# Performance work log

Measured on AMD Instinct MI355X. Metric: run time of the kernel, lower is better.

## Reference

```python
import jax, jax.numpy as jnp
import numpy as np

NUM_EMB = 8192
EMB_DIM = 512
SPAN = 8            # max_span == fixed_segment_size
COMMIT = 0.25
BOUND_W = 0.01


def setup_inputs() -> dict:
    key = jax.random.key(0)
    k_x, k_e, k_w = jax.random.split(key, 3)
    B, T, D = 16, 8192, EMB_DIM
    x = jax.random.normal(k_x, (B, T, D), dtype=jnp.float32)
    emb = jax.random.normal(k_e, (NUM_EMB, D), dtype=jnp.float32) * 0.02
    Wb = jax.random.normal(k_w, (D, 1), dtype=jnp.float32) * 0.02
    bb = jnp.zeros((1,), dtype=jnp.float32)
    return {"x": x, "emb": emb, "Wb": Wb, "bb": bb}


def reference(x, emb, Wb, bb):
    # Eval-mode forward of AdaptiveTemporalVQ (no gumbel sampling, no EMA update).
    B, T, D = x.shape
    # boundary predictor: Linear(D, 1) -> squeeze
    boundary_logits = (x @ Wb)[..., 0] + bb[0]                      # [B, T]
    boundaries = (jax.nn.sigmoid(boundary_logits) > 0.5).astype(x.dtype)

    num_segments = (T + SPAN - 1) // SPAN
    pad = num_segments * SPAN - T
    x_p = jnp.pad(x, ((0, 0), (0, pad), (0, 0))) if pad > 0 else x
    # temporal mean pooling over fixed segments
    pooled = x_p.reshape(B, num_segments, SPAN, D).mean(axis=2)      # [B, S, D]

    # --- VectorQuantizer ---
    flat = pooled.reshape(-1, D)                                     # [N, D]
    dist = (jnp.sum(flat ** 2, axis=1, keepdims=True)
            + jnp.sum(emb ** 2, axis=1)
            - 2.0 * flat @ emb.T)                                    # [N, K]
    idx = jnp.argmin(dist, axis=1)                                   # [N]
    quantized = emb[idx].reshape(B, num_segments, D)                 # codebook gather

    e_latent_loss = jnp.mean((jax.lax.stop_gradient(quantized) - pooled) ** 2)
    vq_loss = COMMIT * e_latent_loss
    # straight-through estimator
    q_st = pooled + jax.lax.stop_gradient(quantized - pooled)

    # expand each segment code back over its SPAN timesteps
    q_exp = jnp.broadcast_to(q_st[:, :, None, :], (B, num_segments, SPAN, D))
    quantized_out = q_exp.reshape(B, num_segments * SPAN, D)[:, :T, :]
    idx_seg = idx.reshape(B, num_segments)
    idx_out = jnp.broadcast_to(idx_seg[:, :, None], (B, num_segments, SPAN))
    idx_out = idx_out.reshape(B, num_segments * SPAN)[:, :T]

    target_rate = jnp.float32(1.0 / SPAN)
    boundary_loss = (boundaries.mean() - target_rate) ** 2
    total_loss = vq_loss + BOUND_W * boundary_loss
    return quantized_out, total_loss, idx_out, boundaries
```

## Files before the change

### kernel.cpp

```cpp
#include <hip/hip_runtime.h>

#define B_    16
#define T_    8192
#define D_    512
#define K_    8192
#define S_    1024
#define N_    16384
#define NBT   131072

#define LOSS_OFF 67108864
#define IDX_OFF  67108865
#define BND_OFF  67239937

typedef __bf16 bf16x8 __attribute__((ext_vector_type(8)));
typedef float  f32x4  __attribute__((ext_vector_type(4)));

__device__ __forceinline__ unsigned int fsort(float f){
  unsigned int u = __float_as_uint(f);
  return (u & 0x80000000u) ? ~u : (u | 0x80000000u);
}
__device__ __forceinline__ float funsort(unsigned int su){
  unsigned int u = (su & 0x80000000u) ? (su ^ 0x80000000u) : ~su;
  return __uint_as_float(u);
}
__device__ __forceinline__ unsigned short f2bf(float f){
  unsigned int u = __float_as_uint(f);
  return (unsigned short)((u + 0x7fffu + ((u >> 16) & 1u)) >> 16);
}
__device__ __forceinline__ void gload16(const void* g, void* l){
  __builtin_amdgcn_global_load_lds((const __attribute__((address_space(1))) void*)g,
                                   (__attribute__((address_space(3))) void*)l, 16, 0, 0);
}

#define VMW12() asm volatile("s_waitcnt vmcnt(12)" ::: "memory")
#define VMW8()  asm volatile("s_waitcnt vmcnt(8)"  ::: "memory")
#define VMW4()  asm volatile("s_waitcnt vmcnt(4)"  ::: "memory")
#define VMW0()  asm volatile("s_waitcnt vmcnt(0)"  ::: "memory")
#define LGKW()  asm volatile("s_waitcnt lgkmcnt(0)" ::: "memory")
#define BAR()   asm volatile("s_barrier" ::: "memory")

__global__ void k_embnorm(const float4* __restrict__ emb4, float* __restrict__ enorm,
                          unsigned short* __restrict__ embh, int* __restrict__ cnt){
  if(blockIdx.x == 0 && threadIdx.x == 0) *cnt = 0;
  const int wid  = (blockIdx.x * blockDim.x + threadIdx.x) >> 6;
  const int lane = threadIdx.x & 63;
  float4 a = emb4[wid * 128 + (lane << 1)];
  float4 b = emb4[wid * 128 + (lane << 1) + 1];
  float s = a.x*a.x + a.y*a.y + a.z*a.z + a.w*a.w
          + b.x*b.x + b.y*b.y + b.z*b.z + b.w*b.w;
  #pragma unroll
  for(int off = 32; off; off >>= 1) s += __shfl_xor(s, off);
  if(lane == 0) enorm[wid] = s;
  unsigned short* dst = embh + ((size_t)wid << 9) + (lane << 3);
  *(ushort4*)(dst)     = make_ushort4(f2bf(a.x), f2bf(a.y), f2bf(a.z), f2bf(a.w));
  *(ushort4*)(dst + 4) = make_ushort4(f2bf(b.x), f2bf(b.y), f2bf(b.z), f2bf(b.w));
}

__launch_bounds__(256)
__global__ void k_prep(const float4* __restrict__ x4, const float4* __restrict__ wb4,
                       const float* __restrict__ bb, float4* __restrict__ pooled4,
                       unsigned short* __restrict__ pooledh, float* __restrict__ bnd,
                       int* __restrict__ cnt){
  __shared__ double ld[4][8][8];
  const int tid  = threadIdx.x;
  const int row0 = blockIdx.x << 5;
  const double bbv = (double)bb[0];
  #pragma unroll
  for(int it = 0; it < 2; it++){
    const int slot  = (it << 8) + tid;
    const int seg_l = slot >> 7;
    const int c4    = slot & 127;
    const float4 w  = wb4[c4];
    const float4* src = x4 + ((size_t)(row0 + (seg_l << 3)) * 128 + c4);
    float4 acc = src[0];
    double p[8];
    p[0] = (double)acc.x*w.x + (double)acc.y*w.y + (double)acc.z*w.z + (double)acc.w*w.w;
    #pragma unroll
    for(int t = 1; t < 8; t++){
      const float4 v = src[(size_t)t * 128];
      acc.x += v.x; acc.y += v.y; acc.z += v.z; acc.w += v.w;
      p[t] = (double)v.x*w.x + (double)v.y*w.y + (double)v.z*w.z + (double)v.w*w.w;
    }
    acc.x *= 0.125f; acc.y *= 0.125f; acc.z *= 0.125f; acc.w *= 0.125f;
    const int u = ((blockIdx.x << 2) + seg_l) * 128 + c4;
    pooled4[u] = acc;
    *(ushort4*)(pooledh + ((size_t)u << 2)) =
        make_ushort4(f2bf(acc.x), f2bf(acc.y), f2bf(acc.z), f2bf(acc.w));
    #pragma unroll
    for(int t = 0; t < 8; t++){
      #pragma unroll
      for(int off = 1; off < 16; off <<= 1) p[t] += __shfl_xor(p[t], off);
    }
    if((c4 & 15) == 0){
      #pragma unroll
      for(int t = 0; t < 8; t++) ld[seg_l][t][c4 >> 4] = p[t];
    }
  }
  __syncthreads();
  if(tid < 32){
    const double* q = ld[tid >> 3][tid & 7];
    double s = bbv;
    #pragma unroll
    for(int h = 0; h < 8; h++) s += q[h];
    const bool f = s > 0.0;
    bnd[row0 + tid] = f ? 1.0f : 0.0f;
    const unsigned long long m = __ballot(f);
    if(tid == 0) atomicAdd(cnt, (int)__popcll(m));
  }
}

__launch_bounds__(512)
__global__ void k_distx(const unsigned short* __restrict__ Ah,
                        const unsigned short* __restrict__ Bh,
                        const float* __restrict__ enorm,
                        unsigned long long* __restrict__ cand64){
  __shared__ __align__(16) unsigned short smem[65536];

  const int tid  = threadIdx.x;
  const int w    = tid >> 6, lane = tid & 63;
  const int wm   = w >> 2,  wn   = w & 3;
  const int c    = lane & 15, q  = lane >> 4;

  const int bid   = blockIdx.x;
  const int xcd   = bid & 7;
  const int local = bid >> 3;
  const int row_t = (xcd << 3) + (local & 7);
  const int col_t = local >> 3;
  const int rowbase = row_t << 8;
  const int colbase = col_t << 8;

  f32x4 acc[8][4];
  #pragma unroll
  for(int i = 0; i < 8; i++)
    #pragma unroll
    for(int j = 0; j < 4; j++) acc[i][j] = (f32x4){0.f, 0.f, 0.f, 0.f};

  const int sr  = tid >> 2;
  const int cg  = (((tid & 3) ^ ((tid >> 3) & 3)) << 3);
  const int wbase = w << 9;

  const unsigned short* As0 = Ah + (size_t)(rowbase + sr)       * 512 + cg;
  const unsigned short* As1 = Ah + (size_t)(rowbase + 128 + sr) * 512 + cg;
  const unsigned short* Bs0 = Bh + (size_t)(colbase + sr)       * 512 + cg;
  const unsigned short* Bs1 = Bh + (size_t)(colbase + 128 + sr) * 512 + cg;

  const int ch = ((q ^ ((c >> 1) & 3)) << 3);

  #define STAGE(tt) do{                                                   \
    const int bb_ = ((tt) & 3) << 14;                                     \
    const size_t ko_ = (size_t)(tt) << 5;                                 \
    gload16(As0 + ko_, &smem[bb_ + wbase]);                               \
    gload16(As1 + ko_, &smem[bb_ + 4096  + wbase]);                       \
    gload16(Bs0 + ko_, &smem[bb_ + 8192  + wbase]);                       \
    gload16(Bs1 + ko_, &smem[bb_ + 12288 + wbase]);                       \
  }while(0)

  #define COMPUTE(tt) do{                                                 \
    const int bb_ = ((tt) & 3) << 14;                                     \
    bf16x8 af[8], bg[4];                                                  \
    _Pragma("unroll")                                                     \
    for(int i = 0; i < 8; i++)                                            \
      af[i] = *(const bf16x8*)&smem[bb_ + (wm*128 + i*16 + c)*32 + ch];   \
    _Pragma("unroll")                                                     \
    for(int j = 0; j < 4; j++)                                            \
      bg[j] = *(const bf16x8*)&smem[bb_ + 8192 + (wn*64 + j*16 + c)*32 + ch]; \
    __builtin_amdgcn_s_setprio(1);                                        \
    _Pragma("unroll")                                                     \
    for(int i = 0; i < 8; i++)                                            \
      _Pragma("unroll")                                                   \
      for(int j = 0; j < 4; j++)                                          \
        acc[i][j] = __builtin_amdgcn_mfma_f32_16x16x32_bf16(af[i], bg[j], acc[i][j], 0, 0, 0); \
    __builtin_amdgcn_s_setprio(0);                                        \
  }while(0)

  STAGE(0); STAGE(1); STAGE(2);

  #pragma unroll 1
  for(int t = 0; t < 13; ++t){
    STAGE(t + 3);
    VMW12(); BAR();
    COMPUTE(t);
    LGKW(); BAR();
  }
  VMW8(); BAR(); COMPUTE(13); LGKW(); BAR();
  VMW4(); BAR(); COMPUTE(14); LGKW(); BAR();
  VMW0(); BAR(); COMPUTE(15);

  #undef STAGE
  #undef COMPUTE

  float en[4];
  #pragma unroll
  for(int j = 0; j < 4; j++) en[j] = enorm[colbase + wn*64 + j*16 + c];

  #pragma unroll
  for(int i = 0; i < 8; i++){
    #pragma unroll
    for(int r = 0; r < 4; r++){
      unsigned int k1 = 0xffffffffu, k2 = 0xffffffffu;
      #pragma unroll
      for(int j = 0; j < 4; j++){
        const float d = fmaf(-2.0f, acc[i][j][r], en[j]);
        const unsigned int col = (unsigned int)(colbase + wn*64 + j*16 + c);
        const unsigned int key = (fsort(d) & 0xffffe000u) | col;
        if(key < k1){ k2 = k1; k1 = key; } else if(key < k2){ k2 = key; }
      }
      #pragma unroll
      for(int off = 1; off < 16; off <<= 1){
        const unsigned int o1 = __shfl_xor(k1, off);
        const unsigned int o2 = __shfl_xor(k2, off);
        if(o1 < k1){ k2 = min(k1, o2); k1 = o1; }
        else       { k2 = min(k2, o1); }
      }
      if(c == 0){
        const int row = rowbase + wm*128 + i*16 + (q << 2) + r;
        cand64[((size_t)row << 7) + (col_t << 2) + wn] =
            ((unsigned long long)k2 << 32) | k1;
      }
    }
  }
}

__launch_bounds__(256)
__global__ void k_fixup(const float* __restrict__ pooled, const float* __restrict__ emb,
                        const unsigned long long* __restrict__ cand64,
                        int* __restrict__ idxf, double* __restrict__ part){
  const int lane = threadIdx.x & 63, wv = threadIdx.x >> 6;
  const int row = (blockIdx.x << 2) + wv;
  const ulonglong2* cr = (const ulonglong2*)(cand64 + ((size_t)row << 7));
  const ulonglong2 v = cr[lane];
  unsigned int ks[4];
  ks[0] = (unsigned int)v.x; ks[1] = (unsigned int)(v.x >> 32);
  ks[2] = (unsigned int)v.y; ks[3] = (unsigned int)(v.y >> 32);
  unsigned int mn = min(min(ks[0], ks[1]), min(ks[2], ks[3]));
  #pragma unroll
  for(int off = 32; off; off >>= 1) mn = min(mn, (unsigned int)__shfl_xor(mn, off));
  const float thr = funsort(mn & 0xffffe000u) + 0.01f;

  double bestd = 1e300; int besti = 0x7fffffff;
  const float4* p4 = (const float4*)(pooled + ((size_t)row << 9));
  const float4 pa = p4[lane << 1], pb = p4[(lane << 1) + 1];
  #pragma unroll
  for(int g = 0; g < 4; g++){
    const bool flag = funsort(ks[g] & 0xffffe000u) <= thr;
    unsigned long long mask = __ballot(flag);
    while(mask){
      const int l = __ffsll(mask) - 1;
      mask &= mask - 1;
      const int code = (int)(__shfl(ks[g], l) & 0x1fffu);
      const float4* e4 = (const float4*)(emb + ((size_t)code << 9));
      const float4 ea = e4[lane << 1], eb = e4[(lane << 1) + 1];
      double s = 0.0, d;
      d = (double)pa.x - ea.x; s += d * d;  d = (double)pa.y - ea.y; s += d * d;
      d = (double)pa.z - ea.z; s += d * d;  d = (double)pa.w - ea.w; s += d * d;
      d = (double)pb.x - eb.x; s += d * d;  d = (double)pb.y - eb.y; s += d * d;
      d = (double)pb.z - eb.z; s += d * d;  d = (double)pb.w - eb.w; s += d * d;
      #pragma unroll
      for(int off = 32; off; off >>= 1) s += __shfl_xor(s, off);
      if(s < bestd || (s == bestd && code < besti)){ bestd = s; besti = code; }
    }
  }
  __shared__ double se[4];
  if(lane == 0){ idxf[row] = besti; se[wv] = bestd; }
  __syncthreads();
  if(threadIdx.x == 0) part[blockIdx.x] = se[0] + se[1] + se[2] + se[3];
}

__global__ void k_loss(const double* __restrict__ part, const int* __restrict__ cnt,
                       float* __restrict__ out_loss){
  const int tid = threadIdx.x;
  double s = 0.0;
  for(int i = tid; i < 4096; i += 256) s += part[i];
  #pragma unroll
  for(int off = 32; off; off >>= 1) s += __shfl_xor(s, off);
  __shared__ double sb[4];
  if((tid & 63) == 0) sb[tid >> 6] = s;
  __syncthreads();
  if(tid == 0){
    const double e  = sb[0] + sb[1] + sb[2] + sb[3];
    const double el = e / (double)((size_t)N_ * 512);
    const double bm = (double)(*cnt) / 131072.0 - 0.125;
    const double loss = 0.25 * el + 0.01 * bm * bm;
    *out_loss = (float)loss;
  }
}

__launch_bounds__(256)
__global__ void k_expand(const float4* __restrict__ emb4, const int* __restrict__ idxf,
                         float4* __restrict__ q4, float* __restrict__ idxo){
  const int lane = threadIdx.x & 63, wv = threadIdx.x >> 6;
  const int seg = (blockIdx.x << 2) + wv;
  const int idx = idxf[seg];
  const float4 a = emb4[idx * 128 + (lane << 1)];
  const float4 b = emb4[idx * 128 + (lane << 1) + 1];
  float4* dst = q4 + ((size_t)seg << 10);
  #pragma unroll
  for(int t = 0; t < 8; t++){
    dst[t * 128 + (lane << 1)]     = a;
    dst[t * 128 + (lane << 1) + 1] = b;
  }
  if(lane < 8) idxo[(seg << 3) + lane] = (float)idx;
}

extern "C" void kernel_launch(void* const* d_in, const int* in_sizes, int n_in,
                              void* d_out, int out_size, void* d_ws, size_t ws_size,
                              hipStream_t stream){
  const float* x   = (const float*)d_in[0];
  const float* emb = (const float*)d_in[1];
  const float* wb  = (const float*)d_in[2];
  const float* bb  = (const float*)d_in[3];
  float* out = (float*)d_out;

  char* ws = (char*)d_ws;
  int*    cnt   = (int*)(ws + 0);
  double* part  = (double*)(ws + 64);
  float*  enorm = (float*)(ws + 32832);
  int*    idxf  = (int*)(ws + 65600);

  float*              pooled  = (float*)d_out;
  unsigned long long* cand64  = (unsigned long long*)((char*)d_out + (48ull  << 20));
  unsigned short*     pooledh = (unsigned short*)((char*)d_out + (80ull  << 20));
  unsigned short*     embh    = (unsigned short*)((char*)d_out + (100ull << 20));

  float* bnd   = out + BND_OFF;
  float* idxo  = out + IDX_OFF;
  float* lossp = out + LOSS_OFF;

  hipLaunchKernelGGL(k_embnorm, dim3(2048),  dim3(256), 0, stream, (const float4*)emb, enorm, embh, cnt);
  hipLaunchKernelGGL(k_prep,    dim3(4096),  dim3(256), 0, stream, (const float4*)x, (const float4*)wb,
                     bb, (float4*)pooled, pooledh, bnd, cnt);
  hipLaunchKernelGGL(k_distx,   dim3(2048),  dim3(512), 0, stream, pooledh, embh, enorm, cand64);
  hipLaunchKernelGGL(k_fixup,   dim3(4096),  dim3(256), 0, stream, pooled, emb, cand64, idxf, part);
  hipLaunchKernelGGL(k_loss,    dim3(1),     dim3(256), 0, stream, part, cnt, lossp);
  hipLaunchKernelGGL(k_expand,  dim3(4096),  dim3(256), 0, stream, (const float4*)emb, idxf, (float4*)d_out, idxo);
}
```

Measured before the change: 710.9 us.

## Split GEMM main loop into two half-tile phases interleaving loads with MFMA

Restructures the bf16 distance GEMM main loop so each K-step runs as two phases, each computing half of the A rows. The global-to-LDS loads for the A and B tiles of step t+3 are split across the two phases and issued alongside the LDS fragment reads. The aim is to hold fewer A fragments in registers at once and to overlap load issue with MFMA work more finely. In exchange it adds extra barriers per iteration and more complex wait-count bookkeeping, which could stall the pipeline.

```diff
diff --git a/kernel.cpp b/kernel.cpp
--- a/kernel.cpp
+++ b/kernel.cpp
@@ -32,7 +32,6 @@
                                    (__attribute__((address_space(3))) void*)l, 16, 0, 0);
 }
 
-#define VMW12() asm volatile("s_waitcnt vmcnt(12)" ::: "memory")
 #define VMW8()  asm volatile("s_waitcnt vmcnt(8)"  ::: "memory")
 #define VMW4()  asm volatile("s_waitcnt vmcnt(4)"  ::: "memory")
 #define VMW0()  asm volatile("s_waitcnt vmcnt(0)"  ::: "memory")
@@ -146,48 +145,68 @@
 
   const int ch = ((q ^ ((c >> 1) & 3)) << 3);
 
-  #define STAGE(tt) do{                                                   \
-    const int bb_ = ((tt) & 3) << 14;                                     \
-    const size_t ko_ = (size_t)(tt) << 5;                                 \
-    gload16(As0 + ko_, &smem[bb_ + wbase]);                               \
-    gload16(As1 + ko_, &smem[bb_ + 4096  + wbase]);                       \
-    gload16(Bs0 + ko_, &smem[bb_ + 8192  + wbase]);                       \
-    gload16(Bs1 + ko_, &smem[bb_ + 12288 + wbase]);                       \
+  bf16x8 af[4], bg[4];
+
+  #define SA(tt) do{ const int sb_ = ((tt) & 3) << 14; const size_t ko_ = (size_t)(tt) << 5; \
+    gload16(As0 + ko_, &smem[sb_ + wbase]);                                                  \
+    gload16(As1 + ko_, &smem[sb_ + 4096  + wbase]); }while(0)
+  #define SB(tt) do{ const int sb_ = ((tt) & 3) << 14; const size_t ko_ = (size_t)(tt) << 5; \
+    gload16(Bs0 + ko_, &smem[sb_ + 8192  + wbase]);                                          \
+    gload16(Bs1 + ko_, &smem[sb_ + 12288 + wbase]); }while(0)
+
+  #define PHASE_A(tt, DOST) do{                                             \
+    const int bb_ = ((tt) & 3) << 14;                                       \
+    _Pragma("unroll")                                                       \
+    for(int j = 0; j < 4; j++)                                              \
+      bg[j] = *(const bf16x8*)&smem[bb_ + 8192 + (wn*64 + j*16 + c)*32 + ch]; \
+    _Pragma("unroll")                                                       \
+    for(int i = 0; i < 4; i++)                                              \
+      af[i] = *(const bf16x8*)&smem[bb_ + (wm*128 + i*16 + c)*32 + ch];     \
+    if(DOST) SA((tt) + 3);                                                  \
+    BAR(); LGKW();                                                          \
+    __builtin_amdgcn_s_setprio(1);                                          \
+    _Pragma("unroll")                                                       \
+    for(int i = 0; i < 4; i++)                                              \
+      _Pragma("unroll")                                                     \
+      for(int j = 0; j < 4; j++)                                            \
+        acc[i][j] = __builtin_amdgcn_mfma_f32_16x16x32_bf16(af[i], bg[j], acc[i][j], 0, 0, 0); \
+    __builtin_amdgcn_s_setprio(0);                                          \
+    BAR();                                                                  \
   }while(0)
 
-  #define COMPUTE(tt) do{                                                 \
-    const int bb_ = ((tt) & 3) << 14;                                     \
-    bf16x8 af[8], bg[4];                                                  \
-    _Pragma("unroll")                                                     \
-    for(int i = 0; i < 8; i++)                                            \
-      af[i] = *(const bf16x8*)&smem[bb_ + (wm*128 + i*16 + c)*32 + ch];   \
-    _Pragma("unroll")                                                     \
-    for(int j = 0; j < 4; j++)                                            \
-      bg[j] = *(const bf16x8*)&smem[bb_ + 8192 + (wn*64 + j*16 + c)*32 + ch]; \
-    __builtin_amdgcn_s_setprio(1);                                        \
-    _Pragma("unroll")                                                     \
-    for(int i = 0; i < 8; i++)                                            \
-      _Pragma("unroll")                                                   \
-      for(int j = 0; j < 4; j++)                                          \
-        acc[i][j] = __builtin_amdgcn_mfma_f32_16x16x32_bf16(af[i], bg[j], acc[i][j], 0, 0, 0); \
-    __builtin_amdgcn_s_setprio(0);                                        \
+  #define PHASE_B(tt, DOST) do{                                             \
+    const int bb_ = ((tt) & 3) << 14;                                       \
+    _Pragma("unroll")                                                       \
+    for(int i = 0; i < 4; i++)                                              \
+      af[i] = *(const bf16x8*)&smem[bb_ + (wm*128 + (i+4)*16 + c)*32 + ch]; \
+    if(DOST) SB((tt) + 3);                                                  \
+    BAR(); LGKW();                                                          \
+    __builtin_amdgcn_s_setprio(1);                                          \
+    _Pragma("unroll")                                                       \
+    for(int i = 0; i < 4; i++)                                              \
+      _Pragma("unroll")                                                     \
+      for(int j = 0; j < 4; j++)                                            \
+        acc[i+4][j] = __builtin_amdgcn_mfma_f32_16x16x32_bf16(af[i], bg[j], acc[i+4][j], 0, 0, 0); \
+    __builtin_amdgcn_s_setprio(0);                                          \
   }while(0)
 
-  STAGE(0); STAGE(1); STAGE(2);
+  SA(0); SB(0); SA(1); SB(1); SA(2); SB(2);
+  VMW8(); BAR();
 
   #pragma unroll 1
   for(int t = 0; t < 13; ++t){
-    STAGE(t + 3);
-    VMW12(); BAR();
-    COMPUTE(t);
-    LGKW(); BAR();
-  }
-  VMW8(); BAR(); COMPUTE(13); LGKW(); BAR();
-  VMW4(); BAR(); COMPUTE(14); LGKW(); BAR();
-  VMW0(); BAR(); COMPUTE(15);
-
-  #undef STAGE
-  #undef COMPUTE
+    PHASE_A(t, 1);
+    PHASE_B(t, 1);
+    VMW8(); BAR();
+  }
+  PHASE_A(13, 0); PHASE_B(13, 0); VMW4(); BAR();
+  PHASE_A(14, 0); PHASE_B(14, 0); VMW0(); BAR();
+  PHASE_A(15, 0); PHASE_B(15, 0);
+
+  #undef SA
+  #undef SB
+  #undef PHASE_A
+  #undef PHASE_B
 
   float en[4];
   #pragma unroll
```

After: 705.7 us. Within noise of the previous version (-0.7%).

## Replace LDS-staged GEMM pipeline with direct global-to-register double-buffered loads

Applied to the files above, without the earlier changes.

The distance GEMM kernel no longer stages A/B tiles through shared memory with global_load_lds, barriers and waitcnt pipelining. Each wave now loads its MFMA fragments directly from global memory into registers with two-stage double buffering, and launch bounds request two blocks per CU. This removes LDS traffic and barriers but loses intra-block data reuse, since each wave refetches rows that other waves share, so it leans on L1/L2 bandwidth and raises register pressure.

```diff
diff --git a/kernel.cpp b/kernel.cpp
--- a/kernel.cpp
+++ b/kernel.cpp
@@ -27,17 +27,9 @@
   unsigned int u = __float_as_uint(f);
   return (unsigned short)((u + 0x7fffu + ((u >> 16) & 1u)) >> 16);
 }
-__device__ __forceinline__ void gload16(const void* g, void* l){
-  __builtin_amdgcn_global_load_lds((const __attribute__((address_space(1))) void*)g,
-                                   (__attribute__((address_space(3))) void*)l, 16, 0, 0);
-}
-
-#define VMW12() asm volatile("s_waitcnt vmcnt(12)" ::: "memory")
-#define VMW8()  asm volatile("s_waitcnt vmcnt(8)"  ::: "memory")
-#define VMW4()  asm volatile("s_waitcnt vmcnt(4)"  ::: "memory")
-#define VMW0()  asm volatile("s_waitcnt vmcnt(0)"  ::: "memory")
-#define LGKW()  asm volatile("s_waitcnt lgkmcnt(0)" ::: "memory")
-#define BAR()   asm volatile("s_barrier" ::: "memory")
+
+#define SETP1()    __builtin_amdgcn_s_setprio(1)
+#define SETP0()    __builtin_amdgcn_s_setprio(0)
 
 __global__ void k_embnorm(const float4* __restrict__ emb4, float* __restrict__ enorm,
                           unsigned short* __restrict__ embh, int* __restrict__ cnt){
@@ -109,13 +101,11 @@
   }
 }
 
-__launch_bounds__(512)
+__launch_bounds__(512, 2)
 __global__ void k_distx(const unsigned short* __restrict__ Ah,
                         const unsigned short* __restrict__ Bh,
                         const float* __restrict__ enorm,
                         unsigned long long* __restrict__ cand64){
-  __shared__ __align__(16) unsigned short smem[65536];
-
   const int tid  = threadIdx.x;
   const int w    = tid >> 6, lane = tid & 63;
   const int wm   = w >> 2,  wn   = w & 3;
@@ -135,59 +125,41 @@
     #pragma unroll
     for(int j = 0; j < 4; j++) acc[i][j] = (f32x4){0.f, 0.f, 0.f, 0.f};
 
-  const int sr  = tid >> 2;
-  const int cg  = (((tid & 3) ^ ((tid >> 3) & 3)) << 3);
-  const int wbase = w << 9;
-
-  const unsigned short* As0 = Ah + (size_t)(rowbase + sr)       * 512 + cg;
-  const unsigned short* As1 = Ah + (size_t)(rowbase + 128 + sr) * 512 + cg;
-  const unsigned short* Bs0 = Bh + (size_t)(colbase + sr)       * 512 + cg;
-  const unsigned short* Bs1 = Bh + (size_t)(colbase + 128 + sr) * 512 + cg;
-
-  const int ch = ((q ^ ((c >> 1) & 3)) << 3);
-
-  #define STAGE(tt) do{                                                   \
-    const int bb_ = ((tt) & 3) << 14;                                     \
-    const size_t ko_ = (size_t)(tt) << 5;                                 \
-    gload16(As0 + ko_, &smem[bb_ + wbase]);                               \
-    gload16(As1 + ko_, &smem[bb_ + 4096  + wbase]);                       \
-    gload16(Bs0 + ko_, &smem[bb_ + 8192  + wbase]);                       \
-    gload16(Bs1 + ko_, &smem[bb_ + 12288 + wbase]);                       \
-  }while(0)
-
-  #define COMPUTE(tt) do{                                                 \
-    const int bb_ = ((tt) & 3) << 14;                                     \
-    bf16x8 af[8], bg[4];                                                  \
-    _Pragma("unroll")                                                     \
-    for(int i = 0; i < 8; i++)                                            \
-      af[i] = *(const bf16x8*)&smem[bb_ + (wm*128 + i*16 + c)*32 + ch];   \
-    _Pragma("unroll")                                                     \
-    for(int j = 0; j < 4; j++)                                            \
-      bg[j] = *(const bf16x8*)&smem[bb_ + 8192 + (wn*64 + j*16 + c)*32 + ch]; \
-    __builtin_amdgcn_s_setprio(1);                                        \
-    _Pragma("unroll")                                                     \
-    for(int i = 0; i < 8; i++)                                            \
-      _Pragma("unroll")                                                   \
-      for(int j = 0; j < 4; j++)                                          \
-        acc[i][j] = __builtin_amdgcn_mfma_f32_16x16x32_bf16(af[i], bg[j], acc[i][j], 0, 0, 0); \
-    __builtin_amdgcn_s_setprio(0);                                        \
-  }while(0)
-
-  STAGE(0); STAGE(1); STAGE(2);
+  const unsigned short* Ap = Ah + (size_t)(rowbase + wm*128 + c) * 512 + q*8;
+  const unsigned short* Bp = Bh + (size_t)(colbase + wn*64 + c) * 512 + q*8;
+
+  bf16x8 a0[8], b0[4], a1[8], b1[4];
+
+  #define LDA(dst, kb) do{ _Pragma("unroll")                                   \
+    for(int i = 0; i < 8; i++)                                                 \
+      dst[i] = *(const bf16x8*)(Ap + (size_t)i*8192 + (kb)); }while(0)
+  #define LDB(dst, kb) do{ _Pragma("unroll")                                   \
+    for(int j = 0; j < 4; j++)                                                 \
+      dst[j] = *(const bf16x8*)(Bp + (size_t)j*8192 + (kb)); }while(0)
+  #define MM(af, bg) do{ SETP1(); _Pragma("unroll")                            \
+    for(int i = 0; i < 8; i++) _Pragma("unroll")                               \
+      for(int j = 0; j < 4; j++)                                               \
+        acc[i][j] = __builtin_amdgcn_mfma_f32_16x16x32_bf16(                   \
+            af[i], bg[j], acc[i][j], 0, 0, 0);                                 \
+    SETP0(); }while(0)
+
+  LDA(a0, 0);  LDB(b0, 0);
+  LDA(a1, 32); LDB(b1, 32);
 
   #pragma unroll 1
-  for(int t = 0; t < 13; ++t){
-    STAGE(t + 3);
-    VMW12(); BAR();
-    COMPUTE(t);
-    LGKW(); BAR();
-  }
-  VMW8(); BAR(); COMPUTE(13); LGKW(); BAR();
-  VMW4(); BAR(); COMPUTE(14); LGKW(); BAR();
-  VMW0(); BAR(); COMPUTE(15);
-
-  #undef STAGE
-  #undef COMPUTE
+  for(int u = 0; u < 7; ++u){
+    const int kb = u << 6;
+    MM(a0, b0);
+    LDA(a0, kb + 64); LDB(b0, kb + 64);
+    MM(a1, b1);
+    LDA(a1, kb + 96); LDB(b1, kb + 96);
+  }
+  MM(a0, b0);
+  MM(a1, b1);
+
+  #undef LDA
+  #undef LDB
+  #undef MM
 
   float en[4];
   #pragma unroll
```

After: 925.7 us. 30.2% more time.
